# Performance work log

Hardware: AMD Instinct MI355X
Metric: run time of the kernel (lower is better)

The kernel has to match this reference:

```python
import jax, jax.numpy as jnp
import numpy as np

GMAX = 1.0   # args.gmax
GMIN = 0.01  # args.gmin
EPS = 0.1    # args.e_train


def setup_inputs() -> dict:
    key = jax.random.key(0)
    k1, k2, k3, k4 = jax.random.split(key, 4)
    N, B, NIN, NOUT, E = 8, 32, 128, 128, 1024
    # analog signals live in [0, 1]
    a_previous = jax.random.uniform(k1, (N, B, NIN, E), dtype=jnp.float32)
    # conductance params (clamped to [-gmax, gmax] in forward)
    theta = jax.random.uniform(k2, (NIN + 2, NOUT), dtype=jnp.float32) * 2.0 - 1.0
    # per-replica multiplicative noise seed in [0, 1); forward maps to 1 +- eps
    noise = jax.random.uniform(k3, (N, NIN + 2, NOUT), dtype=jnp.float32)
    # printed-tanh activation params eta = [offset, scale, shift, slope]
    eta = jnp.array([0.0, 1.0, 0.0, 1.0], dtype=jnp.float32) + 0.1 * jax.random.normal(k4, (4,), dtype=jnp.float32)
    return {"a_previous": a_previous, "theta": theta, "noise": noise, "eta": eta}


def reference(a_previous, theta, noise, eta):
    sg = jax.lax.stop_gradient
    # theta property: clamp + gmin pruning with straight-through estimator
    t = jnp.clip(theta, -GMAX, GMAX)
    t = jnp.where(jnp.abs(t) < GMIN, 0.0, t)
    theta_eff = sg(t) + theta - sg(theta)
    # theta_noisy: replicate over N with multiplicative uniform noise in [1-eps, 1+eps]
    theta_noisy = theta_eff[None, :, :] * ((noise * 2.0 - 1.0) * EPS + 1.0)  # [N, M, O], M = n_in+2
    # W: abs-normalized conductances per output column group
    abs_tn = jnp.abs(theta_noisy)
    W = abs_tn / (jnp.sum(abs_tn, axis=1, keepdims=True) + 1e-10)
    # sign masks (constants w.r.t. grad: values fully overwritten in torch)
    pos = sg((theta_noisy >= 0.0).astype(theta_noisy.dtype))
    neg = 1.0 - pos
    # a: [N, B, n_in, E] -> [N, B, E, n_in]; append ones and zeros columns
    a_r = jnp.transpose(a_previous, (0, 1, 3, 2))
    ones = jnp.ones(a_r.shape[:3] + (1,), a_r.dtype)
    zeros = jnp.zeros_like(ones)
    a_ext = jnp.concatenate([a_r, ones, zeros], axis=3)  # [N, B, E, M]
    # INV: unipolar complement; zero the last (zeros) column after inversion
    a_neg = (1.0 - a_ext).at[..., -1].set(0.0)
    # split-sign MAC: z [N, B, E, n_out]
    z = (jnp.einsum('nbem,nmo->nbeo', a_ext, W * pos)
         + jnp.einsum('nbem,nmo->nbeo', a_neg, W * neg))
    # printed tanh activation
    act = eta[0] + eta[1] * jnp.tanh((z - eta[2]) * eta[3])
    # back to [N, B, n_out, E]
    return jnp.transpose(act, (0, 1, 3, 2))
```

## Files before the change

### kernel.cpp

```cpp
#include <hip/hip_runtime.h>
#include <hip/hip_bf16.h>
#include <stdint.h>

#define N_REP 8
#define BATCH 32
#define NIN   128
#define NOUT  128
#define EDIM  1024
#define MDIM  130
#define SROW  36
#define SLICE (16 * SROW)

typedef __attribute__((ext_vector_type(8))) short short8;
typedef __attribute__((ext_vector_type(4))) float f32x4;

__device__ __forceinline__ unsigned short f2bf(float f) {
    union { float f; uint32_t u; } v;
    v.f = f;
    uint32_t u = v.u;
    uint32_t r = u + 0x7fffu + ((u >> 16) & 1u);
    return (unsigned short)(r >> 16);
}

__device__ __forceinline__ uint32_t pk2bf(float lo, float hi) {
    __hip_bfloat162 h = __float22bfloat162_rn(make_float2(lo, hi));
    uint32_t d;
    __builtin_memcpy(&d, &h, 4);
    return d;
}

__global__ __launch_bounds__(64)
void prep_kernel(const float* __restrict__ theta,
                 const float* __restrict__ noise,
                 unsigned short* __restrict__ Sg,
                 float* __restrict__ biasg) {
    const int n = blockIdx.x >> 7;
    const int o = blockIdx.x & 127;
    const int lane = threadIdx.x;

    const float* nb = noise + (size_t)n * MDIM * NOUT + o;
    auto tn_at = [&](int m) -> float {
        float t = theta[m * NOUT + o];
        t = fminf(fmaxf(t, -1.f), 1.f);
        if (fabsf(t) < 0.01f) t = 0.f;
        return t * fmaf(nb[m * NOUT], 0.2f, 0.9f);
    };

    const float t0 = tn_at(lane);
    const float t1 = tn_at(lane + 64);
    const float t2 = (lane < 2) ? tn_at(128 + lane) : 0.f;

    float s = fabsf(t0) + fabsf(t1) + fabsf(t2);
#pragma unroll
    for (int d = 1; d < 64; d <<= 1) s += __shfl_xor(s, d, 64);
    const float inv = 1.f / (s + 1e-10f);

    const float w0 = fabsf(t0) * inv, w1 = fabsf(t1) * inv;
    unsigned short* srow = Sg + ((size_t)n * NOUT + o) * NIN;
    srow[lane]      = f2bf(t0 >= 0.f ? w0 : -w0);
    srow[lane + 64] = f2bf(t1 >= 0.f ? w1 : -w1);

    float b = (t0 < 0.f ? w0 : 0.f) + (t1 < 0.f ? w1 : 0.f);
    if (lane == 0 && t2 >= 0.f) b += fabsf(t2) * inv;
#pragma unroll
    for (int d = 1; d < 64; d <<= 1) b += __shfl_xor(b, d, 64);
    if (lane == 0) biasg[n * NOUT + o] = b;
}

__global__ __launch_bounds__(256, 3)
void gemm_kernel(const float* __restrict__ a,
                 const unsigned short* __restrict__ Sg,
                 const float* __restrict__ biasg,
                 const float* __restrict__ eta,
                 float* __restrict__ out) {
    __shared__ uint32_t Alds[4][2][SLICE];
    const int bid  = blockIdx.x;
    const int nb   = bid >> 3;
    const int n    = nb >> 5;
    const int eb   = bid & 7;
    const int tid  = threadIdx.x;
    const int lane = tid & 63;
    const int wv   = tid >> 6;
    const int r    = lane & 15;
    const int q    = lane >> 4;
    const int e0   = (eb << 7) + (wv << 5);

    const int mp_l = lane >> 2;
    const int ec   = (lane & 3) << 2;
    const float* abase = a + (size_t)nb * (NIN * EDIM) + e0 + ec;
    uint32_t* L = &Alds[wv][0][0];

    float4 va[2], vb[2];
    auto issue = [&](int t) {
        const float* gp = abase + (size_t)(2 * mp_l + (t << 5)) * EDIM;
#pragma unroll
        for (int i = 0; i < 2; ++i) {
            va[i] = *(const float4*)(gp + (i << 4));
            vb[i] = *(const float4*)(gp + EDIM + (i << 4));
        }
    };
    auto pack_write = [&](int buf) {
#pragma unroll
        for (int i = 0; i < 2; ++i) {
            uint4 d;
            d.x = pk2bf(va[i].x, vb[i].x);
            d.y = pk2bf(va[i].y, vb[i].y);
            d.z = pk2bf(va[i].z, vb[i].z);
            d.w = pk2bf(va[i].w, vb[i].w);
            *(uint4*)&L[buf * SLICE + mp_l * SROW + ec + (i << 4)] = d;
        }
    };

    float e0f = eta[0], e1f = eta[1], e2f = eta[2], e3f = eta[3];
    asm volatile("" : "+v"(e0f), "+v"(e1f), "+v"(e2f), "+v"(e3f));

    f32x4 acc[8][2];
#pragma unroll
    for (int fo = 0; fo < 8; ++fo)
#pragma unroll
        for (int fe = 0; fe < 2; ++fe)
            acc[fo][fe] = (f32x4){0.f, 0.f, 0.f, 0.f};

    const unsigned short* sbase = Sg + ((size_t)(n * NOUT) << 7) + (q << 3);

    issue(0);
    pack_write(0);
    issue(1);

#pragma unroll
    for (int t = 0; t < 4; ++t) {
        const int buf = t & 1;
        short8 af[2];
#pragma unroll
        for (int fe = 0; fe < 2; ++fe) {
            uint32_t d[4];
#pragma unroll
            for (int jj = 0; jj < 4; ++jj)
                d[jj] = L[buf * SLICE + ((q << 2) + jj) * SROW + (fe << 4) + r];
            __builtin_memcpy(&af[fe], d, 16);
        }
#pragma unroll
        for (int fo2 = 0; fo2 < 4; ++fo2) {
            const short8 s0 = *(const short8*)(sbase + ((size_t)((fo2 << 5) + r) << 7) + (t << 5));
            const short8 s1 = *(const short8*)(sbase + ((size_t)((fo2 << 5) + 16 + r) << 7) + (t << 5));
#pragma unroll
            for (int fe = 0; fe < 2; ++fe) {
                acc[fo2 * 2][fe] = __builtin_amdgcn_mfma_f32_16x16x32_bf16(
                    af[fe], s0, acc[fo2 * 2][fe], 0, 0, 0);
                acc[fo2 * 2 + 1][fe] = __builtin_amdgcn_mfma_f32_16x16x32_bf16(
                    af[fe], s1, acc[fo2 * 2 + 1][fe], 0, 0, 0);
            }
        }
        if (t < 3) {
            pack_write(buf ^ 1);
            if (t < 2) issue(t + 2);
        }
    }

    float* obase = out + (size_t)nb * (NOUT * EDIM) + e0;
#pragma unroll
    for (int fo = 0; fo < 8; ++fo) {
        const float bv = biasg[n * NOUT + (fo << 4) + r];
        float* orow = obase + (size_t)((fo << 4) + r) * EDIM;
#pragma unroll
        for (int fe = 0; fe < 2; ++fe) {
            f32x4 res;
#pragma unroll
            for (int i = 0; i < 4; ++i) {
                const float z = acc[fo][fe][i] + bv;
                const float y = (z - e2f) * e3f;
                const float ex = __expf(2.f * y);
                const float th = 1.f - 2.f * __builtin_amdgcn_rcpf(ex + 1.f);
                res[i] = fmaf(e1f, th, e0f);
            }
            *(f32x4*)(orow + (fe << 4) + (q << 2)) = res;
        }
    }
}

extern "C" void kernel_launch(void* const* d_in, const int* in_sizes, int n_in,
                              void* d_out, int out_size, void* d_ws, size_t ws_size,
                              hipStream_t stream) {
    const float* a     = (const float*)d_in[0];
    const float* theta = (const float*)d_in[1];
    const float* noise = (const float*)d_in[2];
    const float* eta   = (const float*)d_in[3];
    float* out = (float*)d_out;

    unsigned short* Sg = (unsigned short*)d_ws;
    float* biasg = (float*)((char*)d_ws + (size_t)N_REP * NOUT * NIN * sizeof(unsigned short));

    prep_kernel<<<N_REP * NOUT, 64, 0, stream>>>(theta, noise, Sg, biasg);
    gemm_kernel<<<N_REP * BATCH * 8, 256, 0, stream>>>(a, Sg, biasg, eta, out);
}
```

Before: 270.2 us.

## Use 512-thread blocks with shared LDS tile and wide row-contiguous A loads

Restructures the GEMM kernel so each 512-thread block covers 256 E positions. Every wave now loads contiguous 1KB rows of the activation tensor (each lane reads a float4) instead of scattered 64-byte pieces. The packed bf16 data goes into a block-shared, E-major LDS tile padded to 17 words per row, and block-wide barriers replace the old per-wave private buffers. This is meant to improve global load coalescing and DRAM efficiency, at the cost of __syncthreads stalls and possible LDS bank conflicts from the strided scalar stores.

```diff
diff --git a/kernel.cpp b/kernel.cpp
--- a/kernel.cpp
+++ b/kernel.cpp
@@ -8,8 +8,9 @@
 #define NOUT  128
 #define EDIM  1024
 #define MDIM  130
-#define SROW  36
-#define SLICE (16 * SROW)
+#define ETB   256
+#define LROW  17
+#define NSL   4
 
 typedef __attribute__((ext_vector_type(8))) short short8;
 typedef __attribute__((ext_vector_type(4))) float f32x4;
@@ -67,52 +68,41 @@
     if (lane == 0) biasg[n * NOUT + o] = b;
 }
 
-__global__ __launch_bounds__(256, 3)
+__global__ __launch_bounds__(512, 4)
 void gemm_kernel(const float* __restrict__ a,
                  const unsigned short* __restrict__ Sg,
                  const float* __restrict__ biasg,
                  const float* __restrict__ eta,
                  float* __restrict__ out) {
-    __shared__ uint32_t Alds[4][2][SLICE];
+    __shared__ uint32_t Alds[2][ETB][LROW];
     const int bid  = blockIdx.x;
-    const int nb   = bid >> 3;
+    const int nb   = bid >> 2;
     const int n    = nb >> 5;
-    const int eb   = bid & 7;
+    const int et   = bid & 3;
     const int tid  = threadIdx.x;
     const int lane = tid & 63;
     const int wv   = tid >> 6;
     const int r    = lane & 15;
     const int q    = lane >> 4;
-    const int e0   = (eb << 7) + (wv << 5);
 
-    const int mp_l = lane >> 2;
-    const int ec   = (lane & 3) << 2;
-    const float* abase = a + (size_t)nb * (NIN * EDIM) + e0 + ec;
-    uint32_t* L = &Alds[wv][0][0];
+    const int eL = lane << 2;
+    const float* gA = a + (size_t)nb * (NIN * EDIM) + et * ETB + eL;
 
-    float4 va[2], vb[2];
-    auto issue = [&](int t) {
-        const float* gp = abase + (size_t)(2 * mp_l + (t << 5)) * EDIM;
-#pragma unroll
-        for (int i = 0; i < 2; ++i) {
-            va[i] = *(const float4*)(gp + (i << 4));
-            vb[i] = *(const float4*)(gp + EDIM + (i << 4));
-        }
+    f32x4 va0, va1, vb0, vb1;
+    auto issue = [&](int s) {
+        const float* gp = gA + (size_t)(s * 32 + (wv << 1)) * EDIM;
+        va0 = *(const f32x4*)(gp);
+        va1 = *(const f32x4*)(gp + EDIM);
+        vb0 = *(const f32x4*)(gp + 16 * EDIM);
+        vb1 = *(const f32x4*)(gp + 17 * EDIM);
     };
     auto pack_write = [&](int buf) {
 #pragma unroll
-        for (int i = 0; i < 2; ++i) {
-            uint4 d;
-            d.x = pk2bf(va[i].x, vb[i].x);
-            d.y = pk2bf(va[i].y, vb[i].y);
-            d.z = pk2bf(va[i].z, vb[i].z);
-            d.w = pk2bf(va[i].w, vb[i].w);
-            *(uint4*)&L[buf * SLICE + mp_l * SROW + ec + (i << 4)] = d;
+        for (int j = 0; j < 4; ++j) {
+            Alds[buf][eL + j][wv]     = pk2bf(va0[j], va1[j]);
+            Alds[buf][eL + j][wv + 8] = pk2bf(vb0[j], vb1[j]);
         }
     };
-
-    float e0f = eta[0], e1f = eta[1], e2f = eta[2], e3f = eta[3];
-    asm volatile("" : "+v"(e0f), "+v"(e1f), "+v"(e2f), "+v"(e3f));
 
     f32x4 acc[8][2];
 #pragma unroll
@@ -125,18 +115,21 @@
 
     issue(0);
     pack_write(0);
-    issue(1);
+    __syncthreads();
 
 #pragma unroll
-    for (int t = 0; t < 4; ++t) {
+    for (int t = 0; t < NSL; ++t) {
         const int buf = t & 1;
+        if (t + 1 < NSL) issue(t + 1);
+
         short8 af[2];
 #pragma unroll
         for (int fe = 0; fe < 2; ++fe) {
+            const int e = (wv << 5) + (fe << 4) + r;
             uint32_t d[4];
 #pragma unroll
             for (int jj = 0; jj < 4; ++jj)
-                d[jj] = L[buf * SLICE + ((q << 2) + jj) * SROW + (fe << 4) + r];
+                d[jj] = Alds[buf][e][(q << 2) + jj];
             __builtin_memcpy(&af[fe], d, 16);
         }
 #pragma unroll
@@ -151,13 +144,16 @@
                     af[fe], s1, acc[fo2 * 2 + 1][fe], 0, 0, 0);
             }
         }
-        if (t < 3) {
+
+        if (t + 1 < NSL) {
             pack_write(buf ^ 1);
-            if (t < 2) issue(t + 2);
+            __syncthreads();
         }
     }
 
-    float* obase = out + (size_t)nb * (NOUT * EDIM) + e0;
+    float e0f = eta[0], e1f = eta[1], e2f = eta[2], e3f = eta[3];
+    asm volatile("" : "+v"(e0f), "+v"(e1f), "+v"(e2f), "+v"(e3f));
+    float* obase = out + (size_t)nb * (NOUT * EDIM) + et * ETB + (wv << 5);
 #pragma unroll
     for (int fo = 0; fo < 8; ++fo) {
         const float bv = biasg[n * NOUT + (fo << 4) + r];
@@ -191,5 +187,5 @@
     float* biasg = (float*)((char*)d_ws + (size_t)N_REP * NOUT * NIN * sizeof(unsigned short));
 
     prep_kernel<<<N_REP * NOUT, 64, 0, stream>>>(theta, noise, Sg, biasg);
-    gemm_kernel<<<N_REP * BATCH * 8, 256, 0, stream>>>(a, Sg, biasg, eta, out);
+    gemm_kernel<<<N_REP * BATCH * (EDIM / ETB), 512, 0, stream>>>(a, Sg, biasg, eta, out);
 }
```

New measurement: 258.8 us. -4.2%, faster.
